# Kernel optimization log

Measured on AMD Instinct MI355X. Metric: run time of the kernel, lower is better.

Reference implementation:

```python
import jax, jax.numpy as jnp
import numpy as np

B, N, E, H = 2, 2048, 768, 12
D = E // H          # head_dim = 64
G = 16              # gate_dim
LN_EPS = 1e-5


def setup_inputs() -> dict:
    key = jax.random.key(0)
    ks = jax.random.split(key, 8)
    s = E ** -0.5
    x = jax.random.normal(ks[0], (B, N, E), jnp.float32)
    # per-head negative decay slopes (ALiBi/TNL-style)
    log_slope = -(2.0 ** (-8.0 * (jnp.arange(H, dtype=jnp.float32) + 1.0) / H))
    Wq = jax.random.normal(ks[1], (E, E), jnp.float32) * s
    Wk = jax.random.normal(ks[2], (E, E), jnp.float32) * s
    Wv = jax.random.normal(ks[3], (E, E), jnp.float32) * s
    Wo = jax.random.normal(ks[4], (E, E), jnp.float32) * s
    Wg1 = jax.random.normal(ks[5], (E, G), jnp.float32) * s
    Wg2 = jax.random.normal(ks[6], (G, E), jnp.float32) * (G ** -0.5)
    ln_w = jnp.ones((E,), jnp.float32)
    ln_b = jnp.zeros((E,), jnp.float32)
    return {"x": x, "log_slope": log_slope, "Wq": Wq, "Wk": Wk, "Wv": Wv,
            "Wo": Wo, "Wg1": Wg1, "Wg2": Wg2, "ln_w": ln_w, "ln_b": ln_b}


def _layernorm(x, w, b):
    mu = jnp.mean(x, axis=-1, keepdims=True)
    var = jnp.mean(jnp.square(x - mu), axis=-1, keepdims=True)
    return (x - mu) * jax.lax.rsqrt(var + LN_EPS) * w + b


def reference(x, log_slope, Wq, Wk, Wv, Wo, Wg1, Wg2, ln_w, ln_b):
    b, n, e = x.shape
    h = log_slope.shape[0]
    d = e // h
    silu = jax.nn.silu
    q = silu(x @ Wq).reshape(b, n, h, d).transpose(0, 2, 1, 3)  # b h n d
    k = silu(x @ Wk).reshape(b, n, h, d).transpose(0, 2, 1, 3)
    v = silu(x @ Wv).reshape(b, n, h, d).transpose(0, 2, 1, 3)

    # exp-decay causal mask: exp(log_slope * (i - j)) for i >= j, else 0
    idx = jnp.arange(n, dtype=jnp.float32)
    diff = idx[:, None] - idx[None, :]                    # n x m
    keep = diff >= 0
    decay = jnp.where(keep,
                      jnp.exp(log_slope[:, None, None] * jnp.maximum(diff, 0.0)),
                      0.0)                                # h n m

    energy = jnp.einsum('bhnd,bhmd->bhnm', q, k) * decay  # b h n m
    out = jnp.einsum('bhnm,bhmd->bhnd', energy, v)        # b h n d
    out = out.transpose(0, 2, 1, 3).reshape(b, n, e)

    gate = jax.nn.sigmoid((x @ Wg1) @ Wg2)                # low-rank output gate
    out = out * gate
    out = out @ Wo
    out = _layernorm(out, ln_w, ln_b)                     # norm_pos='post'
    return out
```

## Files before the change

### kernel.cpp

```cpp
#include <hip/hip_runtime.h>
#include <stdint.h>

#define BB 2
#define NN 2048
#define EE 768
#define HH 12
#define DD 64
#define GG 16

typedef unsigned short u16;
typedef unsigned int u32;
typedef __attribute__((ext_vector_type(8))) short short8;
typedef __attribute__((ext_vector_type(4))) float f32x4;
typedef __attribute__((ext_vector_type(4))) unsigned short u16x4;

__device__ __forceinline__ u16 f2bf(float f) {
  union { float f; u32 u; } a; a.f = f;
  u32 r = a.u + 0x7FFFu + ((a.u >> 16) & 1u);
  return (u16)(r >> 16);
}
__device__ __forceinline__ float bf2f(short s) {
  union { u32 u; float f; } a; a.u = ((u32)(u16)s) << 16; return a.f;
}

__device__ __forceinline__ float silu_f(float v) { return v / (1.f + __expf(-v)); }

__device__ __forceinline__ void gload16(const u16* g, char* l) {
  __builtin_amdgcn_global_load_lds(
      (const __attribute__((address_space(1))) void*)(g),
      (__attribute__((address_space(3))) void*)(l), 16, 0, 0);
}

template<int ROWS>
__device__ __forceinline__ void stage_tile(const u16* __restrict__ gb, int ld, int row0, int col0,
                                           char* lds, int tid) {
  int wid = tid >> 6;
#pragma unroll
  for (int it = 0; it < ROWS / 32; ++it) {
    int c = it * 256 + tid;
    int r = c >> 3;
    int g = (c & 7) ^ (r & 7);
    gload16(gb + (size_t)(row0 + r) * ld + col0 + g * 8,
            lds + (it * 256 + wid * 64) * 16);
  }
}

__device__ __forceinline__ void stage_S(const u16* __restrict__ base, char* lds, int tid, int plane) {
  int wid = tid >> 6;
#pragma unroll
  for (int it = 0; it < 2; ++it) {
    int c = it * 256 + tid;
    int r = c >> 3;
    int g = (c & 7) ^ (r & 7);
    gload16(base + (r >> 4) * 2048 + plane * 1024 + (r & 15) * 64 + g * 8,
            lds + (it * 256 + wid * 64) * 16);
  }
}

__device__ __forceinline__ short8 read_frag(const char* lds, int row, int gk) {
  return *(const short8*)(lds + (((row << 3) | (gk ^ (row & 7))) << 4));
}

__device__ __forceinline__ short8 scale_frag(short8 f, float sc) {
  short8 o;
#pragma unroll
  for (int i = 0; i < 8; ++i) o[i] = (short)f2bf(bf2f(f[i]) * sc);
  return o;
}

__global__ __launch_bounds__(256) void prep_kernel(const float* __restrict__ x,
    const float* __restrict__ Wq, const float* __restrict__ Wk, const float* __restrict__ Wv,
    const float* __restrict__ Wo, const float* __restrict__ Wg1,
    u16* __restrict__ xb, u16* __restrict__ Wqt, u16* __restrict__ Wkt,
    u16* __restrict__ Wvt, u16* __restrict__ Wot, float* __restrict__ tgp) {
  __shared__ float tb[64][65];
  int gx = blockIdx.x, tid = threadIdx.x;
  if (gx < 3072) {
    int i = gx * 256 + tid;
    float4 v = ((const float4*)x)[i];
    u16x4 o;
    o.x = f2bf(v.x); o.y = f2bf(v.y); o.z = f2bf(v.z); o.w = f2bf(v.w);
    ((u16x4*)xb)[i] = o;
  } else if (gx < 3648) {
    int g2 = gx - 3072;
    int z = g2 / 144, rem = g2 % 144;
    int kx = rem / 12, ny = rem % 12;
    const float* src; u16* dst;
    if (z == 0)      { src = Wq; dst = Wqt; }
    else if (z == 1) { src = Wk; dst = Wkt; }
    else if (z == 2) { src = Wv; dst = Wvt; }
    else             { src = Wo; dst = Wot; }
    int k0 = kx * 64, n0 = ny * 64;
#pragma unroll
    for (int i = 0; i < 16; ++i) {
      int idx = i * 256 + tid;
      int r = idx >> 6, c = idx & 63;
      tb[r][c] = src[(size_t)(k0 + r) * EE + n0 + c];
    }
    __syncthreads();
#pragma unroll
    for (int i = 0; i < 16; ++i) {
      int idx = i * 256 + tid;
      int rn = idx >> 6, ck = idx & 63;
      dst[(size_t)(n0 + rn) * EE + k0 + ck] = f2bf(tb[ck][rn]);
    }
  } else {
    int lane = tid & 63, wid = tid >> 6;
    int m = (gx - 3648) * 4 + wid;
    int col = lane & 15, sl = lane >> 4;
    const float* xr = x + (size_t)m * EE + sl * 192;
    float acc = 0.f;
#pragma unroll 4
    for (int i = 0; i < 48; ++i) {
      float4 xv = ((const float4*)xr)[i];
      int kk = sl * 192 + i * 4;
      acc += xv.x * Wg1[(kk + 0) * GG + col];
      acc += xv.y * Wg1[(kk + 1) * GG + col];
      acc += xv.z * Wg1[(kk + 2) * GG + col];
      acc += xv.w * Wg1[(kk + 3) * GG + col];
    }
    acc += __shfl_down(acc, 32);
    acc += __shfl_down(acc, 16);
    if (lane < 16) tgp[(size_t)m * GG + col] = acc;
  }
}

__global__ __launch_bounds__(256) void qkv_gemm(const u16* __restrict__ xb,
    const u16* __restrict__ Wqt, const u16* __restrict__ Wkt, const u16* __restrict__ Wvt,
    u16* __restrict__ qp, u16* __restrict__ kp, u16* __restrict__ ktp, u16* __restrict__ vtp) {
  __shared__ __attribute__((aligned(16))) char As[8192];
  __shared__ __attribute__((aligned(16))) char Zs[16384];
  int tid = threadIdx.x, lane = tid & 63, wid = tid >> 6;
  int quad = lane >> 4, l15 = lane & 15;
  int m0 = blockIdx.x * 64, n0 = blockIdx.y * 128, w = blockIdx.z;
  const u16* Zt = (w == 0) ? Wqt : (w == 1) ? Wkt : Wvt;
  int wm = wid >> 1, wn = wid & 1;
  f32x4 acc[2][4] = {};
  for (int kt = 0; kt < EE / 64; ++kt) {
    __syncthreads();
    stage_tile<64>(xb, EE, m0, kt * 64, As, tid);
    stage_tile<128>(Zt, EE, n0, kt * 64, Zs, tid);
    __syncthreads();
    short8 af[2][2], bfr[2][4];
#pragma unroll
    for (int ds = 0; ds < 2; ++ds) {
      int gk = ds * 4 + quad;
#pragma unroll
      for (int i = 0; i < 2; ++i)
        af[ds][i] = read_frag(As, wm * 32 + i * 16 + l15, gk);
#pragma unroll
      for (int i = 0; i < 4; ++i)
        bfr[ds][i] = read_frag(Zs, wn * 64 + i * 16 + l15, gk);
    }
#pragma unroll
    for (int mi = 0; mi < 2; ++mi)
#pragma unroll
      for (int ni = 0; ni < 4; ++ni) {
        acc[mi][ni] = __builtin_amdgcn_mfma_f32_16x16x32_bf16(af[0][mi], bfr[0][ni], acc[mi][ni], 0, 0, 0);
        acc[mi][ni] = __builtin_amdgcn_mfma_f32_16x16x32_bf16(af[1][mi], bfr[1][ni], acc[mi][ni], 0, 0, 0);
      }
  }
#pragma unroll
  for (int mi = 0; mi < 2; ++mi) {
    int mbase = m0 + wm * 32 + mi * 16 + (quad << 2);
    int bidx = mbase >> 11, nbase = mbase & 2047;
#pragma unroll
    for (int ni = 0; ni < 4; ++ni) {
      int e = n0 + wn * 64 + ni * 16 + l15;
      int h = e >> 6, d = e & 63;
      u16 v0 = f2bf(silu_f(acc[mi][ni][0]));
      u16 v1 = f2bf(silu_f(acc[mi][ni][1]));
      u16 v2 = f2bf(silu_f(acc[mi][ni][2]));
      u16 v3 = f2bf(silu_f(acc[mi][ni][3]));
      if (w < 2) {
        u16* dst = (w == 0 ? qp : kp) + (size_t)(bidx * HH + h) * NN * DD + d;
        dst[(size_t)(nbase + 0) * DD] = v0;
        dst[(size_t)(nbase + 1) * DD] = v1;
        dst[(size_t)(nbase + 2) * DD] = v2;
        dst[(size_t)(nbase + 3) * DD] = v3;
        if (w == 1) {
          u16x4 pk; pk.x = v0; pk.y = v1; pk.z = v2; pk.w = v3;
          *(u16x4*)(ktp + (size_t)((bidx * HH + h) * DD + d) * NN + nbase) = pk;
        }
      } else {
        u16x4 pk; pk.x = v0; pk.y = v1; pk.z = v2; pk.w = v3;
        *(u16x4*)(vtp + (size_t)((bidx * HH + h) * DD + d) * NN + nbase) = pk;
      }
    }
  }
}

__global__ __launch_bounds__(256) void lstate_kernel(const u16* __restrict__ ktp,
    const u16* __restrict__ vtp, const float* __restrict__ slopes, float* __restrict__ Lst) {
  __shared__ __attribute__((aligned(16))) char KTs[8192];
  __shared__ __attribute__((aligned(16))) char VTs[8192];
  int tid = threadIdx.x, lane = tid & 63, wid = tid >> 6;
  int quad = lane >> 4, l15 = lane & 15;
  int c = blockIdx.x, bh = blockIdx.y, h = bh % HH;
  float slope = slopes[h];
  const u16* ktb = ktp + (size_t)bh * DD * NN;
  const u16* vtb = vtp + (size_t)bh * DD * NN;
  stage_tile<64>(vtb, NN, 0, c * 64, VTs, tid);
  stage_tile<64>(ktb, NN, 0, c * 64, KTs, tid);
  __syncthreads();
  f32x4 acc[4] = {};
  float em = __expf(-slope);
#pragma unroll
  for (int ks = 0; ks < 2; ++ks) {
    int kg = ks * 4 + quad;
    short8 vf = read_frag(VTs, wid * 16 + l15, kg);
    float f = __expf(slope * (float)(64 - kg * 8));
    short8 vdf;
#pragma unroll
    for (int jj = 0; jj < 8; ++jj) { vdf[jj] = (short)f2bf(bf2f(vf[jj]) * f); f *= em; }
#pragma unroll
    for (int dt = 0; dt < 4; ++dt)
      acc[dt] = __builtin_amdgcn_mfma_f32_16x16x32_bf16(
          vdf, read_frag(KTs, dt * 16 + l15, kg), acc[dt], 0, 0, 0);
  }
  float* Lo = Lst + ((size_t)bh * 32 + c) * 4096;
#pragma unroll
  for (int dt = 0; dt < 4; ++dt)
#pragma unroll
    for (int r = 0; r < 4; ++r)
      Lo[(wid * 16 + quad * 4 + r) * 64 + dt * 16 + l15] = acc[dt][r];
}

__global__ __launch_bounds__(256) void scan_kernel(const float* __restrict__ Lst,
    float* __restrict__ Sst, const float* __restrict__ slopes) {
  int g = blockIdx.x, bh = blockIdx.y, h = bh % HH, t = threadIdx.x;
  float D = __expf(slopes[h] * 64.f);
  const float* base = Lst + (size_t)bh * 32 * 4096;
  float* obase = Sst + (size_t)bh * 32 * 4096;
  int off = g * 1024 + t * 4;
  float4 acc = {0.f, 0.f, 0.f, 0.f};
  float4 ring[8];
#pragma unroll
  for (int i = 0; i < 8; ++i) ring[i] = *(const float4*)(base + (size_t)i * 4096 + off);
  for (int c = 0; c < 31; ++c) {
    float4 cur = ring[c & 7];
    if (c + 8 < 31) ring[c & 7] = *(const float4*)(base + (size_t)(c + 8) * 4096 + off);
    acc.x = acc.x * D + cur.x;
    acc.y = acc.y * D + cur.y;
    acc.z = acc.z * D + cur.z;
    acc.w = acc.w * D + cur.w;
    float a[4] = {acc.x, acc.y, acc.z, acc.w};
    u16 hv[4], lv[4];
#pragma unroll
    for (int i = 0; i < 4; ++i) {
      hv[i] = f2bf(a[i]);
      lv[i] = f2bf(a[i] - bf2f((short)hv[i]));
    }
    u16x4 hi, lo;
    hi.x = hv[0]; hi.y = hv[1]; hi.z = hv[2]; hi.w = hv[3];
    lo.x = lv[0]; lo.y = lv[1]; lo.z = lv[2]; lo.w = lv[3];
    u16* sb = (u16*)(obase + (size_t)c * 4096);
    int wo = g * 2048 + (t >> 4) * 64 + (t & 15) * 4;
    *(u16x4*)(sb + wo) = hi;
    *(u16x4*)(sb + wo + 1024) = lo;
  }
}

__global__ __launch_bounds__(256) void attn_chunk(const u16* __restrict__ qp,
    const u16* __restrict__ kp, const u16* __restrict__ vtp,
    const float* __restrict__ slopes, const float* __restrict__ Sst,
    const float* __restrict__ tgp, const float* __restrict__ Wg2, u16* __restrict__ attnb) {
  __shared__ __attribute__((aligned(16))) char Ks[8192];
  __shared__ __attribute__((aligned(16))) char Vs[8192];
  __shared__ __attribute__((aligned(16))) char Sh[8192];
  __shared__ __attribute__((aligned(16))) char Sl[8192];
  __shared__ __attribute__((aligned(16))) char Ps[4][2304];
  __shared__ float ts[64][16];
  __shared__ float w2[16][64];
  int tid = threadIdx.x, lane = tid & 63, wid = tid >> 6;
  int quad = lane >> 4, l15 = lane & 15;
  int c = blockIdx.x, bh = blockIdx.y, b = bh / HH, h = bh % HH;
  float slope = slopes[h];
  int q0 = c * 64;
  const u16* qbh = qp + (size_t)bh * NN * DD;
  const u16* kbh = kp + (size_t)bh * NN * DD;
  const u16* vbh = vtp + (size_t)bh * DD * NN;

  stage_tile<64>(kbh, DD, q0, 0, Ks, tid);
  stage_tile<64>(vbh, NN, 0, q0, Vs, tid);
  if (c > 0) {
    const u16* sb = (const u16*)(Sst + ((size_t)bh * 32 + (c - 1)) * 4096);
    stage_S(sb, Sh, tid, 0);
    stage_S(sb, Sl, tid, 1);
  }
  {
    float4 tv = *(const float4*)(tgp + ((size_t)(b * NN + q0) + (tid >> 2)) * GG + (tid & 3) * 4);
    *(float4*)&ts[tid >> 2][(tid & 3) * 4] = tv;
    float4 wv = *(const float4*)(Wg2 + (size_t)(tid >> 4) * EE + h * 64 + (tid & 15) * 4);
    *(float4*)&w2[tid >> 4][(tid & 15) * 4] = wv;
  }
  int qrow = q0 + wid * 16 + l15;
  short8 qf0 = *(const short8*)(qbh + (size_t)qrow * DD + (quad << 3));
  short8 qf1 = *(const short8*)(qbh + (size_t)qrow * DD + 32 + (quad << 3));
  __syncthreads();

  f32x4 oacc[4] = {};
  char* Pw = Ps[wid];
  int qbase = q0 + wid * 16 + (quad << 2);

  float t_hi = (float)(q0 + 63);
  float rex[4];
#pragma unroll
  for (int r = 0; r < 4; ++r) rex[r] = __expf(slope * ((float)(qbase + r) - t_hi));
#pragma unroll
  for (int jt = 0; jt < 4; ++jt) {
    f32x4 s = {};
    s = __builtin_amdgcn_mfma_f32_16x16x32_bf16(qf0, read_frag(Ks, jt * 16 + l15, quad), s, 0, 0, 0);
    s = __builtin_amdgcn_mfma_f32_16x16x32_bf16(qf1, read_frag(Ks, jt * 16 + l15, 4 + quad), s, 0, 0, 0);
    int jg = q0 + jt * 16 + l15;
    float cex = __expf(slope * (t_hi - (float)jg));
#pragma unroll
    for (int r = 0; r < 4; ++r) {
      int diff = qbase + r - jg;
      float val = (diff >= 0) ? s[r] * rex[r] * cex : 0.f;
      *(u16*)(Pw + (((quad << 2) + r) * 72 + jt * 16 + l15) * 2) = f2bf(val);
    }
  }
  __asm__ volatile("s_waitcnt lgkmcnt(0)" ::: "memory");
#pragma unroll
  for (int ks = 0; ks < 2; ++ks) {
    short8 pf = *(const short8*)(Pw + l15 * 144 + ks * 64 + (quad << 4));
#pragma unroll
    for (int dt = 0; dt < 4; ++dt) {
      oacc[dt] = __builtin_amdgcn_mfma_f32_16x16x32_bf16(
          pf, read_frag(Vs, dt * 16 + l15, ks * 4 + quad), oacc[dt], 0, 0, 0);
    }
  }

  if (c > 0) {
    int il = wid * 16 + l15;
    float qsc = __expf(slope * (float)il);
    short8 qd0 = scale_frag(qf0, qsc);
    short8 qd1 = scale_frag(qf1, qsc);
#pragma unroll
    for (int dt = 0; dt < 4; ++dt) {
      oacc[dt] = __builtin_amdgcn_mfma_f32_16x16x32_bf16(qd0, read_frag(Sh, dt * 16 + l15, quad), oacc[dt], 0, 0, 0);
      oacc[dt] = __builtin_amdgcn_mfma_f32_16x16x32_bf16(qd1, read_frag(Sh, dt * 16 + l15, 4 + quad), oacc[dt], 0, 0, 0);
      oacc[dt] = __builtin_amdgcn_mfma_f32_16x16x32_bf16(qd0, read_frag(Sl, dt * 16 + l15, quad), oacc[dt], 0, 0, 0);
      oacc[dt] = __builtin_amdgcn_mfma_f32_16x16x32_bf16(qd1, read_frag(Sl, dt * 16 + l15, 4 + quad), oacc[dt], 0, 0, 0);
    }
  }

#pragma unroll
  for (int r = 0; r < 4; ++r) {
    int row = wid * 16 + (quad << 2) + r;
    float gv[4] = {0.f, 0.f, 0.f, 0.f};
#pragma unroll
    for (int g = 0; g < 16; ++g) {
      float tv = ts[row][g];
#pragma unroll
      for (int dt = 0; dt < 4; ++dt) gv[dt] += tv * w2[g][dt * 16 + l15];
    }
#pragma unroll
    for (int dt = 0; dt < 4; ++dt)
      oacc[dt][r] *= 1.f / (1.f + __expf(-gv[dt]));
  }

#pragma unroll
  for (int dt = 0; dt < 4; ++dt)
#pragma unroll
    for (int r = 0; r < 4; ++r) {
      int qi = qbase + r;
      int e = h * 64 + dt * 16 + l15;
      attnb[(size_t)(b * NN + qi) * EE + e] = f2bf(oacc[dt][r]);
    }
}

__global__ __launch_bounds__(256) void wo_gemm(const u16* __restrict__ A, const u16* __restrict__ Zt,
                                               float* __restrict__ Y) {
  __shared__ __attribute__((aligned(16))) char As[8192];
  __shared__ __attribute__((aligned(16))) char Zs[16384];
  int tid = threadIdx.x, lane = tid & 63, wid = tid >> 6;
  int quad = lane >> 4, l15 = lane & 15;
  int m0 = blockIdx.x * 64, n0 = blockIdx.y * 128;
  int wm = wid >> 1, wn = wid & 1;
  f32x4 acc[2][4] = {};
  for (int kt = 0; kt < EE / 64; ++kt) {
    __syncthreads();
    stage_tile<64>(A, EE, m0, kt * 64, As, tid);
    stage_tile<128>(Zt, EE, n0, kt * 64, Zs, tid);
    __syncthreads();
    short8 af[2][2], bfr[2][4];
#pragma unroll
    for (int ds = 0; ds < 2; ++ds) {
      int gk = ds * 4 + quad;
#pragma unroll
      for (int i = 0; i < 2; ++i)
        af[ds][i] = read_frag(As, wm * 32 + i * 16 + l15, gk);
#pragma unroll
      for (int i = 0; i < 4; ++i)
        bfr[ds][i] = read_frag(Zs, wn * 64 + i * 16 + l15, gk);
    }
#pragma unroll
    for (int mi = 0; mi < 2; ++mi)
#pragma unroll
      for (int ni = 0; ni < 4; ++ni) {
        acc[mi][ni] = __builtin_amdgcn_mfma_f32_16x16x32_bf16(af[0][mi], bfr[0][ni], acc[mi][ni], 0, 0, 0);
        acc[mi][ni] = __builtin_amdgcn_mfma_f32_16x16x32_bf16(af[1][mi], bfr[1][ni], acc[mi][ni], 0, 0, 0);
      }
  }
#pragma unroll
  for (int mi = 0; mi < 2; ++mi) {
    int mbase = m0 + wm * 32 + mi * 16 + (quad << 2);
#pragma unroll
    for (int ni = 0; ni < 4; ++ni) {
      int e = n0 + wn * 64 + ni * 16 + l15;
#pragma unroll
      for (int r = 0; r < 4; ++r)
        Y[(size_t)(mbase + r) * EE + e] = acc[mi][ni][r];
    }
  }
}

__global__ __launch_bounds__(256) void ln_kernel(const float* __restrict__ y, const float* __restrict__ w,
    const float* __restrict__ bb, float* __restrict__ out) {
  int m = blockIdx.x, tid = threadIdx.x;
  const float* yr = y + (size_t)m * EE;
  float v0 = yr[tid], v1 = yr[tid + 256], v2 = yr[tid + 512];
  float s = v0 + v1 + v2;
  float s2 = v0 * v0 + v1 * v1 + v2 * v2;
#pragma unroll
  for (int off = 32; off > 0; off >>= 1) {
    s += __shfl_down(s, off);
    s2 += __shfl_down(s2, off);
  }
  __shared__ float ss[4], ssq[4];
  int lane = tid & 63, wid = tid >> 6;
  if (lane == 0) { ss[wid] = s; ssq[wid] = s2; }
  __syncthreads();
  s = ss[0] + ss[1] + ss[2] + ss[3];
  s2 = ssq[0] + ssq[1] + ssq[2] + ssq[3];
  float mu = s * (1.f / 768.f);
  float var = s2 * (1.f / 768.f) - mu * mu;
  float rs = rsqrtf(var + 1e-5f);
  float* orow = out + (size_t)m * EE;
  orow[tid]       = (v0 - mu) * rs * w[tid]       + bb[tid];
  orow[tid + 256] = (v1 - mu) * rs * w[tid + 256] + bb[tid + 256];
  orow[tid + 512] = (v2 - mu) * rs * w[tid + 512] + bb[tid + 512];
}

extern "C" void kernel_launch(void* const* d_in, const int* in_sizes, int n_in,
                              void* d_out, int out_size, void* d_ws, size_t ws_size,
                              hipStream_t stream) {
  (void)in_sizes; (void)n_in; (void)out_size; (void)ws_size;
  const float* x   = (const float*)d_in[0];
  const float* ls  = (const float*)d_in[1];
  const float* Wq  = (const float*)d_in[2];
  const float* Wk  = (const float*)d_in[3];
  const float* Wv  = (const float*)d_in[4];
  const float* Wo  = (const float*)d_in[5];
  const float* Wg1 = (const float*)d_in[6];
  const float* Wg2 = (const float*)d_in[7];
  const float* lnw = (const float*)d_in[8];
  const float* lnb = (const float*)d_in[9];

  char* p = (char*)d_ws;
  u16* xb    = (u16*)(p + 0);
  u16* attnb = (u16*)(p + 0);
  u16* Wqt   = (u16*)(p + 6291456);
  u16* Wkt   = (u16*)(p + 7471104);
  u16* Wvt   = (u16*)(p + 8650752);
  u16* Wot   = (u16*)(p + 9830400);
  u16* qq    = (u16*)(p + 11010048);
  u16* kk    = (u16*)(p + 17301504);
  u16* vt    = (u16*)(p + 23592960);
  float* tg  = (float*)(p + 29884416);
  float* Lst = (float*)(p + 30146560);
  u16* kt2   = (u16*)(p + 42729472);
  float* Sst = (float*)(p + 49020928);
  float* yy  = (float*)(p + 11010048);
  float* out = (float*)d_out;

  hipLaunchKernelGGL(prep_kernel, dim3(4672), dim3(256), 0, stream, x, Wq, Wk, Wv, Wo, Wg1,
                     xb, Wqt, Wkt, Wvt, Wot, tg);
  hipLaunchKernelGGL(qkv_gemm, dim3(64, 6, 3), dim3(256), 0, stream, xb, Wqt, Wkt, Wvt, qq, kk, kt2, vt);
  hipLaunchKernelGGL(lstate_kernel, dim3(32, 24), dim3(256), 0, stream, kt2, vt, ls, Lst);
  hipLaunchKernelGGL(scan_kernel, dim3(4, 24), dim3(256), 0, stream, Lst, Sst, ls);
  hipLaunchKernelGGL(attn_chunk, dim3(32, 24), dim3(256), 0, stream, qq, kk, vt, ls, Sst, tg, Wg2, attnb);
  hipLaunchKernelGGL(wo_gemm, dim3(64, 6), dim3(256), 0, stream, attnb, Wot, yy);
  hipLaunchKernelGGL(ln_kernel, dim3(4096), dim3(256), 0, stream, yy, lnw, lnb, out);
}
```

Baseline: 173.4 us.

## Enlarge QKV GEMM tile, fuse x cast into gate prep, store Wo output as bf16

The QKV GEMM tile grows from 64 to 128 rows, so each wave computes a 64x64 block and B-tile reuse doubles, at the cost of more registers and LDS. The x-to-bf16 conversion moves into the gate-projection blocks, which already read each row of x, so x is read once instead of twice. The Wo GEMM writes its intermediate in bf16 instead of fp32, halving that round trip before LayerNorm but adding rounding error ahead of normalization.

```diff
diff --git a/kernel.cpp b/kernel.cpp
--- a/kernel.cpp
+++ b/kernel.cpp
@@ -75,15 +75,8 @@
     u16* __restrict__ Wvt, u16* __restrict__ Wot, float* __restrict__ tgp) {
   __shared__ float tb[64][65];
   int gx = blockIdx.x, tid = threadIdx.x;
-  if (gx < 3072) {
-    int i = gx * 256 + tid;
-    float4 v = ((const float4*)x)[i];
-    u16x4 o;
-    o.x = f2bf(v.x); o.y = f2bf(v.y); o.z = f2bf(v.z); o.w = f2bf(v.w);
-    ((u16x4*)xb)[i] = o;
-  } else if (gx < 3648) {
-    int g2 = gx - 3072;
-    int z = g2 / 144, rem = g2 % 144;
+  if (gx < 576) {
+    int z = gx / 144, rem = gx % 144;
     int kx = rem / 12, ny = rem % 12;
     const float* src; u16* dst;
     if (z == 0)      { src = Wq; dst = Wqt; }
@@ -106,13 +99,21 @@
     }
   } else {
     int lane = tid & 63, wid = tid >> 6;
-    int m = (gx - 3648) * 4 + wid;
+    int m = (gx - 576) * 4 + wid;
+    const float* xr = x + (size_t)m * EE;
+#pragma unroll
+    for (int j = 0; j < 3; ++j) {
+      float4 v = ((const float4*)xr)[lane + 64 * j];
+      u16x4 o;
+      o.x = f2bf(v.x); o.y = f2bf(v.y); o.z = f2bf(v.z); o.w = f2bf(v.w);
+      ((u16x4*)(xb + (size_t)m * EE))[lane + 64 * j] = o;
+    }
     int col = lane & 15, sl = lane >> 4;
-    const float* xr = x + (size_t)m * EE + sl * 192;
+    const float* xs = xr + sl * 192;
     float acc = 0.f;
 #pragma unroll 4
     for (int i = 0; i < 48; ++i) {
-      float4 xv = ((const float4*)xr)[i];
+      float4 xv = ((const float4*)xs)[i];
       int kk = sl * 192 + i * 4;
       acc += xv.x * Wg1[(kk + 0) * GG + col];
       acc += xv.y * Wg1[(kk + 1) * GG + col];
@@ -128,32 +129,31 @@
 __global__ __launch_bounds__(256) void qkv_gemm(const u16* __restrict__ xb,
     const u16* __restrict__ Wqt, const u16* __restrict__ Wkt, const u16* __restrict__ Wvt,
     u16* __restrict__ qp, u16* __restrict__ kp, u16* __restrict__ ktp, u16* __restrict__ vtp) {
-  __shared__ __attribute__((aligned(16))) char As[8192];
+  __shared__ __attribute__((aligned(16))) char As[16384];
   __shared__ __attribute__((aligned(16))) char Zs[16384];
   int tid = threadIdx.x, lane = tid & 63, wid = tid >> 6;
   int quad = lane >> 4, l15 = lane & 15;
-  int m0 = blockIdx.x * 64, n0 = blockIdx.y * 128, w = blockIdx.z;
+  int m0 = blockIdx.x * 128, n0 = blockIdx.y * 128, w = blockIdx.z;
   const u16* Zt = (w == 0) ? Wqt : (w == 1) ? Wkt : Wvt;
   int wm = wid >> 1, wn = wid & 1;
-  f32x4 acc[2][4] = {};
+  f32x4 acc[4][4] = {};
   for (int kt = 0; kt < EE / 64; ++kt) {
     __syncthreads();
-    stage_tile<64>(xb, EE, m0, kt * 64, As, tid);
+    stage_tile<128>(xb, EE, m0, kt * 64, As, tid);
     stage_tile<128>(Zt, EE, n0, kt * 64, Zs, tid);
     __syncthreads();
-    short8 af[2][2], bfr[2][4];
+    short8 af[2][4], bfr[2][4];
 #pragma unroll
     for (int ds = 0; ds < 2; ++ds) {
       int gk = ds * 4 + quad;
 #pragma unroll
-      for (int i = 0; i < 2; ++i)
-        af[ds][i] = read_frag(As, wm * 32 + i * 16 + l15, gk);
-#pragma unroll
-      for (int i = 0; i < 4; ++i)
+      for (int i = 0; i < 4; ++i) {
+        af[ds][i]  = read_frag(As, wm * 64 + i * 16 + l15, gk);
         bfr[ds][i] = read_frag(Zs, wn * 64 + i * 16 + l15, gk);
-    }
-#pragma unroll
-    for (int mi = 0; mi < 2; ++mi)
+      }
+    }
+#pragma unroll
+    for (int mi = 0; mi < 4; ++mi)
 #pragma unroll
       for (int ni = 0; ni < 4; ++ni) {
         acc[mi][ni] = __builtin_amdgcn_mfma_f32_16x16x32_bf16(af[0][mi], bfr[0][ni], acc[mi][ni], 0, 0, 0);
@@ -161,8 +161,8 @@
       }
   }
 #pragma unroll
-  for (int mi = 0; mi < 2; ++mi) {
-    int mbase = m0 + wm * 32 + mi * 16 + (quad << 2);
+  for (int mi = 0; mi < 4; ++mi) {
+    int mbase = m0 + wm * 64 + mi * 16 + (quad << 2);
     int bidx = mbase >> 11, nbase = mbase & 2047;
 #pragma unroll
     for (int ni = 0; ni < 4; ++ni) {
@@ -372,7 +372,7 @@
 }
 
 __global__ __launch_bounds__(256) void wo_gemm(const u16* __restrict__ A, const u16* __restrict__ Zt,
-                                               float* __restrict__ Y) {
+                                               u16* __restrict__ Y) {
   __shared__ __attribute__((aligned(16))) char As[8192];
   __shared__ __attribute__((aligned(16))) char Zs[16384];
   int tid = threadIdx.x, lane = tid & 63, wid = tid >> 6;
@@ -412,16 +412,16 @@
       int e = n0 + wn * 64 + ni * 16 + l15;
 #pragma unroll
       for (int r = 0; r < 4; ++r)
-        Y[(size_t)(mbase + r) * EE + e] = acc[mi][ni][r];
-    }
-  }
-}
-
-__global__ __launch_bounds__(256) void ln_kernel(const float* __restrict__ y, const float* __restrict__ w,
+        Y[(size_t)(mbase + r) * EE + e] = f2bf(acc[mi][ni][r]);
+    }
+  }
+}
+
+__global__ __launch_bounds__(256) void ln_kernel(const u16* __restrict__ y, const float* __restrict__ w,
     const float* __restrict__ bb, float* __restrict__ out) {
   int m = blockIdx.x, tid = threadIdx.x;
-  const float* yr = y + (size_t)m * EE;
-  float v0 = yr[tid], v1 = yr[tid + 256], v2 = yr[tid + 512];
+  const u16* yr = y + (size_t)m * EE;
+  float v0 = bf2f((short)yr[tid]), v1 = bf2f((short)yr[tid + 256]), v2 = bf2f((short)yr[tid + 512]);
   float s = v0 + v1 + v2;
   float s2 = v0 * v0 + v1 * v1 + v2 * v2;
 #pragma unroll
@@ -473,12 +473,12 @@
   float* Lst = (float*)(p + 30146560);
   u16* kt2   = (u16*)(p + 42729472);
   float* Sst = (float*)(p + 49020928);
-  float* yy  = (float*)(p + 11010048);
+  u16* yy    = (u16*)(p + 11010048);
   float* out = (float*)d_out;
 
-  hipLaunchKernelGGL(prep_kernel, dim3(4672), dim3(256), 0, stream, x, Wq, Wk, Wv, Wo, Wg1,
+  hipLaunchKernelGGL(prep_kernel, dim3(1600), dim3(256), 0, stream, x, Wq, Wk, Wv, Wo, Wg1,
                      xb, Wqt, Wkt, Wvt, Wot, tg);
-  hipLaunchKernelGGL(qkv_gemm, dim3(64, 6, 3), dim3(256), 0, stream, xb, Wqt, Wkt, Wvt, qq, kk, kt2, vt);
+  hipLaunchKernelGGL(qkv_gemm, dim3(32, 6, 3), dim3(256), 0, stream, xb, Wqt, Wkt, Wvt, qq, kk, kt2, vt);
   hipLaunchKernelGGL(lstate_kernel, dim3(32, 24), dim3(256), 0, stream, kt2, vt, ls, Lst);
   hipLaunchKernelGGL(scan_kernel, dim3(4, 24), dim3(256), 0, stream, Lst, Sst, ls);
   hipLaunchKernelGGL(attn_chunk, dim3(32, 24), dim3(256), 0, stream, qq, kk, vt, ls, Sst, tg, Wg2, attnb);
```

Result: faster. 165.0 us (-4.8%).
